# Kernel tuning notes

Measured on AMD Instinct MI355X. Metric: run time of the kernel, lower is better.

Reference implementation:

```python
import jax, jax.numpy as jnp
import numpy as np

N_NODES = 100000
N_EDGES = 1600000
NUM_FEATURES = 256
HIDDEN = 128
NUM_CLASSES = 40


def setup_inputs() -> dict:
    key = jax.random.key(0)
    k1, k2, k3, k4, k5, k6 = jax.random.split(key, 6)
    x = jax.random.normal(k1, (N_NODES, NUM_FEATURES), dtype=jnp.float32)
    edge_index = jax.random.randint(k2, (2, N_EDGES), 0, N_NODES, dtype=jnp.int64)
    # Glorot-like init for weights, zeros-like small bias
    W1 = jax.random.normal(k3, (NUM_FEATURES, HIDDEN), dtype=jnp.float32) / np.sqrt(NUM_FEATURES)
    b1 = jax.random.normal(k4, (HIDDEN,), dtype=jnp.float32) * 0.01
    W2 = jax.random.normal(k5, (HIDDEN, NUM_CLASSES), dtype=jnp.float32) / np.sqrt(HIDDEN)
    b2 = jax.random.normal(k6, (NUM_CLASSES,), dtype=jnp.float32) * 0.01
    return {"x": x, "edge_index": edge_index, "W1": W1, "b1": b1, "W2": W2, "b2": b2}


def _gcn_norm(edge_index, n_nodes):
    # Add self loops, compute symmetric normalization D^-1/2 (A+I) D^-1/2.
    loops = jnp.arange(n_nodes, dtype=edge_index.dtype)
    src = jnp.concatenate([edge_index[0], loops])  # [E + N]
    dst = jnp.concatenate([edge_index[1], loops])
    ones = jnp.ones(src.shape[0], dtype=jnp.float32)
    deg = jax.ops.segment_sum(ones, dst, num_segments=n_nodes)  # in-degree incl. self loop
    dinv = jnp.where(deg > 0, jax.lax.rsqrt(deg), 0.0)
    norm = dinv[src] * dinv[dst]  # [E + N]
    return src, dst, norm


def _gcn_conv(x, src, dst, norm, W, b, n_nodes):
    h = x @ W                       # [N, out] transform first (PyG GCNConv)
    msg = h[src] * norm[:, None]    # [E+N, out] gather + scale
    out = jax.ops.segment_sum(msg, dst, num_segments=n_nodes)  # scatter-add
    return out + b


def reference(x, edge_index, W1, b1, W2, b2):
    n = x.shape[0]
    src, dst, norm = _gcn_norm(edge_index, n)
    h = jax.nn.relu(_gcn_conv(x, src, dst, norm, W1, b1, n))
    # dropout is identity in eval mode
    h = _gcn_conv(h, src, dst, norm, W2, b2, n)
    return jax.nn.log_softmax(h, axis=1)
```

## Files before the change

kernel.cpp:

```cpp
#include <hip/hip_runtime.h>
#include <hip/hip_bf16.h>
#include <math.h>

#define NN 100000
#define NE 1600000
#define NF 256
#define NH 128
#define NC 40
#define NCP 64
#define NC2 48

#define NBINS     ((NN + 255) / 256)
#define BIN_CAP   5120
#define CHUNK_A   4096
#define NB_A      ((NE + CHUNK_A - 1) / CHUNK_A)
#define GEMM1_NB  ((NN + 127) / 128)

#define OFF_CURSOR  200128
#define OFF_DINV    300160
#define OFF_H       3600192
#define OFF_W1T     10000192
#define OFF_W2T     10016576
#define OFF_EBIN    16400192
#define OFF_EREC4   18402112
#define OFF_H2P     20404032

using f32x4  = __attribute__((ext_vector_type(4))) float;
using bf16x8 = __attribute__((ext_vector_type(8))) short;

__device__ inline float2 cvt2(unsigned u) {
    float2 f;
    f.x = __uint_as_float(u << 16);
    f.y = __uint_as_float(u & 0xffff0000u);
    return f;
}

__device__ inline short bfbits(float f) {
    __hip_bfloat16 h = __float2bfloat16(f);
    return *reinterpret_cast<short*>(&h);
}

__device__ inline unsigned pk2(float lo, float hi) {
    return (unsigned)(unsigned short)bfbits(lo) | ((unsigned)(unsigned short)bfbits(hi) << 16);
}

__global__ void initk(int* __restrict__ bin_cursor,
                      const float* __restrict__ W1, __hip_bfloat16* __restrict__ W1t,
                      const float* __restrict__ W2, __hip_bfloat16* __restrict__ W2t) {
    int t = blockIdx.x * blockDim.x + threadIdx.x;
    if (t < NBINS) bin_cursor[t] = t * BIN_CAP;
    if (t < NH * NF) {
        int n = t >> 8;
        int k = t & (NF - 1);
        W1t[t] = __float2bfloat16(W1[(size_t)k * NH + n]);
    }
    if (t < NCP * NH) {
        int n = t >> 7;
        int k = t & (NH - 1);
        W2t[t] = __float2bfloat16((n < NC) ? W2[(size_t)k * NC + n] : 0.f);
    }
}

__global__ __launch_bounds__(1024, 2) void gemm1_passA(
        const int* __restrict__ ei, int* __restrict__ bin_cursor,
        int* __restrict__ ebin,
        const float* __restrict__ X, const __hip_bfloat16* __restrict__ W1t,
        __hip_bfloat16* __restrict__ H) {
    __shared__ __align__(16) int smem[8192];

    const int bi = blockIdx.x / 3;
    const int br = blockIdx.x % 3;

    if (br == 1) {
        int* hist  = smem;
        int* rbase = smem + NBINS;
        int e0 = bi * CHUNK_A;
        int e1 = e0 + CHUNK_A; if (e1 > NE) e1 = NE;
        for (int j = threadIdx.x; j < NBINS; j += 1024) hist[j] = 0;
        __syncthreads();
        for (int p = e0 + threadIdx.x; p < e1; p += 1024)
            atomicAdd(&hist[ei[NE + p] >> 8], 1);
        __syncthreads();
        for (int j = threadIdx.x; j < NBINS; j += 1024) {
            int c = hist[j];
            rbase[j] = c ? atomicAdd(&bin_cursor[j], c) : 0;
        }
        __syncthreads();
        for (int p = e0 + threadIdx.x; p < e1; p += 1024) {
            int s = ei[p];
            int d = ei[NE + p];
            int bb = d >> 8;
            int pos = atomicAdd(&rbase[bb], 1);
            if (pos < (bb + 1) * BIN_CAP)
                ebin[pos] = s | ((d & 255) << 17);
        }
        return;
    }

    short* As = (short*)smem;
    short* Bs = (short*)smem + 8192;

    const int tid  = threadIdx.x;
    const int wave = tid >> 6;
    const int lane = tid & 63;
    const int quad = lane >> 4;
    const int l16  = lane & 15;
    const int wy = wave >> 1, wx = wave & 1;
    const int m0 = (bi * 2 + (br == 2 ? 1 : 0)) * 128;

    const int xrow = tid >> 3, xc4 = tid & 7;
    int gr = m0 + xrow; if (gr > NN - 1) gr = NN - 1;
    const float* xbase = X + (size_t)gr * NF + xc4 * 4;
    const int xdst = xrow * 32 + xc4 * 4;

    f32x4 acc[4] = {};

    auto stageB = [&](int d, int kk) {
        if (wave < 8) {
            int n = tid >> 2, cc = tid & 3;
            const __hip_bfloat16* gp = W1t + (size_t)n * NF + kk + cc * 8;
            __builtin_amdgcn_global_load_lds(
                (const __attribute__((address_space(1))) void*)gp,
                (__attribute__((address_space(3))) void*)&Bs[d * 4096 + wave * 512],
                16, 0, 0);
        }
    };

    {
        f32x4 xr = *(const f32x4*)xbase;
        stageB(0, 0);
        uint2 wpk;
        wpk.x = pk2(xr.x, xr.y);
        wpk.y = pk2(xr.z, xr.w);
        *reinterpret_cast<uint2*>(&As[xdst]) = wpk;
    }
    __syncthreads();

    int cur = 0;
    #pragma unroll
    for (int k0 = 0; k0 < NF; k0 += 32) {
        const bool more = (k0 + 32 < NF);
        f32x4 xn;
        if (more) {
            xn = *(const f32x4*)(xbase + k0 + 32);
            stageB(cur ^ 1, k0 + 32);
        }

        bf16x8 a_frag = *(const bf16x8*)&As[cur * 4096 + (wy * 16 + l16) * 32 + quad * 8];
        bf16x8 b_frag[4];
        #pragma unroll
        for (int ni = 0; ni < 4; ++ni)
            b_frag[ni] = *(const bf16x8*)&Bs[cur * 4096 + (wx * 64 + ni * 16 + l16) * 32 + quad * 8];
        #pragma unroll
        for (int ni = 0; ni < 4; ++ni)
            acc[ni] = __builtin_amdgcn_mfma_f32_16x16x32_bf16(
                a_frag, b_frag[ni], acc[ni], 0, 0, 0);

        if (more) {
            uint2 wpk;
            wpk.x = pk2(xn.x, xn.y);
            wpk.y = pk2(xn.z, xn.w);
            *reinterpret_cast<uint2*>(&As[(cur ^ 1) * 4096 + xdst]) = wpk;
        }
        __syncthreads();
        cur ^= 1;
    }

    #pragma unroll
    for (int v = 0; v < 4; ++v) {
        int r = m0 + wy * 16 + quad * 4 + v;
        if (r < NN) {
            #pragma unroll
            for (int ni = 0; ni < 4; ++ni) {
                int c = wx * 64 + ni * 16 + l16;
                H[(size_t)r * NH + c] = __float2bfloat16(acc[ni][v]);
            }
        }
    }
}

__global__ __launch_bounds__(512) void buildK2(const int* __restrict__ ebin,
                                               const int* __restrict__ bin_cursor,
                                               int2* __restrict__ offr,
                                               float* __restrict__ dinv,
                                               int* __restrict__ erec4) {
    __shared__ int ecache[BIN_CAP];
    __shared__ int hist[256];
    __shared__ int scn[256];
    __shared__ int wsum4[4];

    const int b   = blockIdx.x;
    const int tid = threadIdx.x;
    const int n0  = b << 8;
    const int nodes = (NN - n0 > 256) ? 256 : (NN - n0);
    const int base = b * BIN_CAP;
    int cnt = bin_cursor[b] - base;
    if (cnt > BIN_CAP) cnt = BIN_CAP;

    for (int j = tid; j < 256; j += 512) hist[j] = 0;
    __syncthreads();

    for (int p = tid; p < cnt; p += 512) {
        int e = ebin[base + p];
        ecache[p] = e;
        atomicAdd(&hist[e >> 17], 1);
    }
    __syncthreads();

    int v = 0, s = 0;
    const int lane = tid & 63, wave = tid >> 6;
    if (tid < 256) {
        v = hist[tid];
        s = v;
        #pragma unroll
        for (int off = 1; off < 64; off <<= 1) {
            int u = __shfl_up(s, off, 64);
            if (lane >= off) s += u;
        }
        if (lane == 63) wsum4[wave] = s;
    }
    __syncthreads();
    if (tid == 0) {
        int a = 0;
        #pragma unroll
        for (int w = 0; w < 4; ++w) { int t = wsum4[w]; wsum4[w] = a; a += t; }
    }
    __syncthreads();
    if (tid < 256) {
        int excl = (s - v) + wsum4[wave];
        scn[tid] = excl;
        if (tid < nodes) {
            offr[n0 + tid] = make_int2(base + excl, base + excl + v);
            dinv[n0 + tid] = rsqrtf((float)v + 1.0f);
        }
    }
    __syncthreads();

    for (int p = tid; p < cnt; p += 512) {
        int e = ecache[p];
        int dl = e >> 17;
        int pos = atomicAdd(&scn[dl], 1);
        if (pos < BIN_CAP) erec4[base + pos] = e & 0x1FFFF;
    }
}

__global__ __launch_bounds__(1024, 2) void agg1_gemm2(
        const int2* __restrict__ offr, const int* __restrict__ erec4,
        const float* __restrict__ dinv, const __hip_bfloat16* __restrict__ H,
        const float* __restrict__ b1, const __hip_bfloat16* __restrict__ W2t,
        __hip_bfloat16* __restrict__ H2p) {
    __shared__ __align__(16) short As[128 * 128];
    const int tid  = threadIdx.x;
    const int wave = tid >> 6;
    const int lane = tid & 63;
    const int quad = lane >> 4;
    const int l16  = lane & 15;
    const int grp  = tid >> 4;
    const int m0   = blockIdx.x * 128;
    const char* Hb = (const char*)H;
    const unsigned lb = (unsigned)(l16 << 4);

    #pragma unroll 1
    for (int rd = 0; rd < 2; ++rd) {
        int nl = rd * 64 + grp;
        int node = m0 + nl;
        if (node < NN) {
            int2 be = offr[node];
            int beg = be.x, end = be.y;
            float dls = dinv[node];
            float ac[8] = {};
            for (int p = beg; p < end; p += 4) {
                int s0 = erec4[p];
                int s1 = (p + 1 < end) ? erec4[p + 1] : 0;
                int s2 = (p + 2 < end) ? erec4[p + 2] : 0;
                int s3 = (p + 3 < end) ? erec4[p + 3] : 0;
                float w0 = dinv[s0];
                float w1 = (p + 1 < end) ? dinv[s1] : 0.f;
                float w2 = (p + 2 < end) ? dinv[s2] : 0.f;
                float w3 = (p + 3 < end) ? dinv[s3] : 0.f;
                uint4 h0 = *(const uint4*)(Hb + (((unsigned)s0) << 8) + lb);
                uint4 h1 = *(const uint4*)(Hb + (((unsigned)s1) << 8) + lb);
                uint4 h2 = *(const uint4*)(Hb + (((unsigned)s2) << 8) + lb);
                uint4 h3 = *(const uint4*)(Hb + (((unsigned)s3) << 8) + lb);
                #define ACC8(hv, ww) { \
                    float2 q0 = cvt2(hv.x), q1 = cvt2(hv.y), q2 = cvt2(hv.z), q3 = cvt2(hv.w); \
                    ac[0] += q0.x * (ww); ac[1] += q0.y * (ww); \
                    ac[2] += q1.x * (ww); ac[3] += q1.y * (ww); \
                    ac[4] += q2.x * (ww); ac[5] += q2.y * (ww); \
                    ac[6] += q3.x * (ww); ac[7] += q3.y * (ww); }
                ACC8(h0, w0) ACC8(h1, w1) ACC8(h2, w2) ACC8(h3, w3)
                #undef ACC8
            }
            float sl = dls * dls;
            uint4 hs = *(const uint4*)(Hb + (((unsigned)node) << 8) + lb);
            float2 s0f = cvt2(hs.x), s1f = cvt2(hs.y), s2f = cvt2(hs.z), s3f = cvt2(hs.w);
            const float4* bb = reinterpret_cast<const float4*>(b1 + l16 * 8);
            float4 ba = bb[0], bc = bb[1];
            float o0 = fmaxf(ac[0] * dls + s0f.x * sl + ba.x, 0.f);
            float o1 = fmaxf(ac[1] * dls + s0f.y * sl + ba.y, 0.f);
            float o2 = fmaxf(ac[2] * dls + s1f.x * sl + ba.z, 0.f);
            float o3 = fmaxf(ac[3] * dls + s1f.y * sl + ba.w, 0.f);
            float o4 = fmaxf(ac[4] * dls + s2f.x * sl + bc.x, 0.f);
            float o5 = fmaxf(ac[5] * dls + s2f.y * sl + bc.y, 0.f);
            float o6 = fmaxf(ac[6] * dls + s3f.x * sl + bc.z, 0.f);
            float o7 = fmaxf(ac[7] * dls + s3f.y * sl + bc.w, 0.f);
            uint4 ov;
            ov.x = pk2(o0, o1);
            ov.y = pk2(o2, o3);
            ov.z = pk2(o4, o5);
            ov.w = pk2(o6, o7);
            unsigned cb = lb ^ (((unsigned)nl & 7u) << 4);
            *reinterpret_cast<uint4*>((char*)As + nl * 256 + cb) = ov;
        }
    }

    bf16x8 bfr[4][3];
    if (wave < 8) {
        #pragma unroll
        for (int ks = 0; ks < 4; ++ks)
            #pragma unroll
            for (int ni = 0; ni < 3; ++ni)
                bfr[ks][ni] = *(const bf16x8*)(W2t + (size_t)(ni * 16 + l16) * NH + ks * 32 + quad * 8);
    }

    __syncthreads();
    if (wave >= 8) return;

    f32x4 acc2[3] = {};
    #pragma unroll
    for (int ks = 0; ks < 4; ++ks) {
        int row = wave * 16 + l16;
        unsigned cb = ((unsigned)(ks * 64 + quad * 16)) ^ (((unsigned)row & 7u) << 4);
        bf16x8 afr = *(const bf16x8*)((const char*)As + row * 256 + cb);
        #pragma unroll
        for (int ni = 0; ni < 3; ++ni)
            acc2[ni] = __builtin_amdgcn_mfma_f32_16x16x32_bf16(
                afr, bfr[ks][ni], acc2[ni], 0, 0, 0);
    }

    #pragma unroll
    for (int v = 0; v < 4; ++v) {
        int r = m0 + wave * 16 + quad * 4 + v;
        if (r < NN) {
            #pragma unroll
            for (int ni = 0; ni < 3; ++ni) {
                int c = ni * 16 + l16;
                H2p[(size_t)r * NC2 + c] = __float2bfloat16(acc2[ni][v]);
            }
        }
    }
}

__global__ void agg2_lsm(const int2* __restrict__ offr, const int* __restrict__ erec4,
                         const float* __restrict__ dinv, const __hip_bfloat16* __restrict__ H2p,
                         const float* __restrict__ b2, float* __restrict__ out) {
    int node = (blockIdx.x * blockDim.x + threadIdx.x) >> 4;
    if (node >= NN) return;
    int l16 = threadIdx.x & 15;
    const char* Hb = (const char*)H2p;
    const bool lv = (l16 < 12);
    const unsigned lo = (unsigned)(l16 * 8);
    const uint2 zz = make_uint2(0u, 0u);
    float a0 = 0.f, a1 = 0.f, a2 = 0.f, a3 = 0.f;
    int2 be = offr[node];
    int beg = be.x, end = be.y;
    float di = dinv[node];
    for (int p = beg; p < end; p += 8) {
        int s[8]; float w[8]; uint2 h[8];
        #pragma unroll
        for (int j = 0; j < 8; ++j) s[j] = (p + j < end) ? erec4[p + j] : 0;
        #pragma unroll
        for (int j = 0; j < 8; ++j) w[j] = (p + j < end) ? dinv[s[j]] : 0.f;
        #pragma unroll
        for (int j = 0; j < 8; ++j) h[j] = lv ? *(const uint2*)(Hb + (unsigned)s[j] * 96u + lo) : zz;
        #pragma unroll
        for (int j = 0; j < 8; ++j) {
            float2 q0 = cvt2(h[j].x), q1 = cvt2(h[j].y);
            a0 += q0.x * w[j]; a1 += q0.y * w[j];
            a2 += q1.x * w[j]; a3 += q1.y * w[j];
        }
    }
    float v0, v1, v2, v3;
    bool valid = (l16 < 10);
    if (valid) {
        float sl = di * di;
        uint2 hs = *(const uint2*)(Hb + (unsigned)node * 96u + lo);
        float2 s0f = cvt2(hs.x), s1f = cvt2(hs.y);
        float4 bb = *reinterpret_cast<const float4*>(b2 + l16 * 4);
        v0 = a0 * di + s0f.x * sl + bb.x;
        v1 = a1 * di + s0f.y * sl + bb.y;
        v2 = a2 * di + s1f.x * sl + bb.z;
        v3 = a3 * di + s1f.y * sl + bb.w;
    } else {
        v0 = v1 = v2 = v3 = -INFINITY;
    }
    float m = fmaxf(fmaxf(v0, v1), fmaxf(v2, v3));
    #pragma unroll
    for (int off = 8; off; off >>= 1) m = fmaxf(m, __shfl_xor(m, off, 64));
    float ex = expf(v0 - m) + expf(v1 - m) + expf(v2 - m) + expf(v3 - m);
    #pragma unroll
    for (int off = 8; off; off >>= 1) ex += __shfl_xor(ex, off, 64);
    float ls = logf(ex);
    if (valid) {
        float4 o;
        o.x = v0 - m - ls; o.y = v1 - m - ls;
        o.z = v2 - m - ls; o.w = v3 - m - ls;
        *reinterpret_cast<float4*>(out + (size_t)node * NC + l16 * 4) = o;
    }
}

extern "C" void kernel_launch(void* const* d_in, const int* in_sizes, int n_in,
                              void* d_out, int out_size, void* d_ws, size_t ws_size,
                              hipStream_t stream) {
    const float* x  = (const float*)d_in[0];
    const int*   ei = (const int*)d_in[1];
    const float* W1 = (const float*)d_in[2];
    const float* b1 = (const float*)d_in[3];
    const float* W2 = (const float*)d_in[4];
    const float* b2 = (const float*)d_in[5];
    float* out = (float*)d_out;

    int* wsb = (int*)d_ws;
    int2*  offr       = (int2*)wsb;
    int*   bin_cursor = wsb + OFF_CURSOR;
    float* dinv       = (float*)(wsb + OFF_DINV);
    __hip_bfloat16* H   = (__hip_bfloat16*)(wsb + OFF_H);
    __hip_bfloat16* W1t = (__hip_bfloat16*)(wsb + OFF_W1T);
    __hip_bfloat16* W2t = (__hip_bfloat16*)(wsb + OFF_W2T);
    int* ebin  = wsb + OFF_EBIN;
    int* erec4 = wsb + OFF_EREC4;
    __hip_bfloat16* H2p = (__hip_bfloat16*)(wsb + OFF_H2P);

    initk<<<(NH * NF + 255) / 256, 256, 0, stream>>>(bin_cursor, W1, W1t, W2, W2t);

    gemm1_passA<<<GEMM1_NB + NB_A, 1024, 0, stream>>>(ei, bin_cursor, ebin, x, W1t, H);

    buildK2<<<NBINS, 512, 0, stream>>>(ebin, bin_cursor, offr, dinv, erec4);

    agg1_gemm2<<<(NN + 127) / 128, 1024, 0, stream>>>(offr, erec4, dinv, H, b1, W2t, H2p);

    {
        long long threads = (long long)NN * 16;
        agg2_lsm<<<(unsigned)((threads + 255) / 256), 256, 0, stream>>>(
            offr, erec4, dinv, H2p, b2, out);
    }
}
```

Before: 315.4 us.

## Widen GEMM1 K-step with swizzled LDS, split H2 into aligned tables, enlarge buildK2

GEMM1 now stages 64-wide K tiles with an XOR-swizzled LDS layout, and all 16 waves issue the W1 direct-to-LDS loads. This halves the barrier count and aims to cut LDS bank conflicts, at the cost of doubled shared memory (64KB) in a kernel declared with launch_bounds(1024,2). The layer-2 features are split into a 64-byte table holding 32 columns and a 16-byte table holding 8 columns, so gathers in agg2 hit aligned, cache-line-friendly rows instead of 96-byte rows. buildK2 runs with 1024 threads instead of 512.

```diff
diff --git a/kernel.cpp b/kernel.cpp
--- a/kernel.cpp
+++ b/kernel.cpp
@@ -8,7 +8,6 @@
 #define NH 128
 #define NC 40
 #define NCP 64
-#define NC2 48
 
 #define NBINS     ((NN + 255) / 256)
 #define BIN_CAP   5120
@@ -23,7 +22,8 @@
 #define OFF_W2T     10016576
 #define OFF_EBIN    16400192
 #define OFF_EREC4   18402112
-#define OFF_H2P     20404032
+#define OFF_H2A     20404032
+#define OFF_H2B     22004032
 
 using f32x4  = __attribute__((ext_vector_type(4))) float;
 using bf16x8 = __attribute__((ext_vector_type(8))) short;
@@ -66,7 +66,7 @@
         int* __restrict__ ebin,
         const float* __restrict__ X, const __hip_bfloat16* __restrict__ W1t,
         __hip_bfloat16* __restrict__ H) {
-    __shared__ __align__(16) int smem[8192];
+    __shared__ __align__(16) int smem[16384];
 
     const int bi = blockIdx.x / 3;
     const int br = blockIdx.x % 3;
@@ -98,7 +98,7 @@
     }
 
     short* As = (short*)smem;
-    short* Bs = (short*)smem + 8192;
+    short* Bs = (short*)smem + 16384;
 
     const int tid  = threadIdx.x;
     const int wave = tid >> 6;
@@ -108,59 +108,64 @@
     const int wy = wave >> 1, wx = wave & 1;
     const int m0 = (bi * 2 + (br == 2 ? 1 : 0)) * 128;
 
-    const int xrow = tid >> 3, xc4 = tid & 7;
-    int gr = m0 + xrow; if (gr > NN - 1) gr = NN - 1;
-    const float* xbase = X + (size_t)gr * NF + xc4 * 4;
-    const int xdst = xrow * 32 + xc4 * 4;
+    const int srow = tid >> 3;
+    const int scl  = (tid & 7) ^ (srow & 7);
+    int gr = m0 + srow; if (gr > NN - 1) gr = NN - 1;
+    const float* xbase = X + (size_t)gr * NF + scl * 8;
+    const __hip_bfloat16* wbase = W1t + (size_t)srow * NF + scl * 8;
+    const int ldst = tid * 8;
 
     f32x4 acc[4] = {};
 
     auto stageB = [&](int d, int kk) {
-        if (wave < 8) {
-            int n = tid >> 2, cc = tid & 3;
-            const __hip_bfloat16* gp = W1t + (size_t)n * NF + kk + cc * 8;
-            __builtin_amdgcn_global_load_lds(
-                (const __attribute__((address_space(1))) void*)gp,
-                (__attribute__((address_space(3))) void*)&Bs[d * 4096 + wave * 512],
-                16, 0, 0);
-        }
+        __builtin_amdgcn_global_load_lds(
+            (const __attribute__((address_space(1))) void*)(wbase + kk),
+            (__attribute__((address_space(3))) void*)&Bs[d * 8192 + ldst],
+            16, 0, 0);
     };
 
     {
-        f32x4 xr = *(const f32x4*)xbase;
+        f32x4 x0 = *(const f32x4*)xbase;
+        f32x4 x1 = *(const f32x4*)(xbase + 4);
         stageB(0, 0);
-        uint2 wpk;
-        wpk.x = pk2(xr.x, xr.y);
-        wpk.y = pk2(xr.z, xr.w);
-        *reinterpret_cast<uint2*>(&As[xdst]) = wpk;
+        uint4 w;
+        w.x = pk2(x0.x, x0.y); w.y = pk2(x0.z, x0.w);
+        w.z = pk2(x1.x, x1.y); w.w = pk2(x1.z, x1.w);
+        *reinterpret_cast<uint4*>(&As[ldst]) = w;
     }
     __syncthreads();
 
     int cur = 0;
     #pragma unroll
-    for (int k0 = 0; k0 < NF; k0 += 32) {
-        const bool more = (k0 + 32 < NF);
-        f32x4 xn;
+    for (int k0 = 0; k0 < NF; k0 += 64) {
+        const bool more = (k0 + 64 < NF);
+        f32x4 x0, x1;
         if (more) {
-            xn = *(const f32x4*)(xbase + k0 + 32);
-            stageB(cur ^ 1, k0 + 32);
-        }
-
-        bf16x8 a_frag = *(const bf16x8*)&As[cur * 4096 + (wy * 16 + l16) * 32 + quad * 8];
-        bf16x8 b_frag[4];
-        #pragma unroll
-        for (int ni = 0; ni < 4; ++ni)
-            b_frag[ni] = *(const bf16x8*)&Bs[cur * 4096 + (wx * 64 + ni * 16 + l16) * 32 + quad * 8];
-        #pragma unroll
-        for (int ni = 0; ni < 4; ++ni)
-            acc[ni] = __builtin_amdgcn_mfma_f32_16x16x32_bf16(
-                a_frag, b_frag[ni], acc[ni], 0, 0, 0);
+            x0 = *(const f32x4*)(xbase + k0 + 64);
+            x1 = *(const f32x4*)(xbase + k0 + 68);
+            stageB(cur ^ 1, k0 + 64);
+        }
+
+        #pragma unroll
+        for (int ks = 0; ks < 2; ++ks) {
+            const int ar = wy * 16 + l16;
+            const int ac = (ks * 4 + quad) ^ (ar & 7);
+            bf16x8 a_frag = *(const bf16x8*)&As[cur * 8192 + ar * 64 + ac * 8];
+            #pragma unroll
+            for (int ni = 0; ni < 4; ++ni) {
+                const int brr = wx * 64 + ni * 16 + l16;
+                const int bc  = (ks * 4 + quad) ^ (brr & 7);
+                bf16x8 b_frag = *(const bf16x8*)&Bs[cur * 8192 + brr * 64 + bc * 8];
+                acc[ni] = __builtin_amdgcn_mfma_f32_16x16x32_bf16(
+                    a_frag, b_frag, acc[ni], 0, 0, 0);
+            }
+        }
 
         if (more) {
-            uint2 wpk;
-            wpk.x = pk2(xn.x, xn.y);
-            wpk.y = pk2(xn.z, xn.w);
-            *reinterpret_cast<uint2*>(&As[(cur ^ 1) * 4096 + xdst]) = wpk;
+            uint4 w;
+            w.x = pk2(x0.x, x0.y); w.y = pk2(x0.z, x0.w);
+            w.z = pk2(x1.x, x1.y); w.w = pk2(x1.z, x1.w);
+            *reinterpret_cast<uint4*>(&As[(cur ^ 1) * 8192 + ldst]) = w;
         }
         __syncthreads();
         cur ^= 1;
@@ -179,11 +184,11 @@
     }
 }
 
-__global__ __launch_bounds__(512) void buildK2(const int* __restrict__ ebin,
-                                               const int* __restrict__ bin_cursor,
-                                               int2* __restrict__ offr,
-                                               float* __restrict__ dinv,
-                                               int* __restrict__ erec4) {
+__global__ __launch_bounds__(1024) void buildK2(const int* __restrict__ ebin,
+                                                const int* __restrict__ bin_cursor,
+                                                int2* __restrict__ offr,
+                                                float* __restrict__ dinv,
+                                                int* __restrict__ erec4) {
     __shared__ int ecache[BIN_CAP];
     __shared__ int hist[256];
     __shared__ int scn[256];
@@ -197,10 +202,10 @@
     int cnt = bin_cursor[b] - base;
     if (cnt > BIN_CAP) cnt = BIN_CAP;
 
-    for (int j = tid; j < 256; j += 512) hist[j] = 0;
-    __syncthreads();
-
-    for (int p = tid; p < cnt; p += 512) {
+    if (tid < 256) hist[tid] = 0;
+    __syncthreads();
+
+    for (int p = tid; p < cnt; p += 1024) {
         int e = ebin[base + p];
         ecache[p] = e;
         atomicAdd(&hist[e >> 17], 1);
@@ -236,7 +241,7 @@
     }
     __syncthreads();
 
-    for (int p = tid; p < cnt; p += 512) {
+    for (int p = tid; p < cnt; p += 1024) {
         int e = ecache[p];
         int dl = e >> 17;
         int pos = atomicAdd(&scn[dl], 1);
@@ -248,7 +253,7 @@
         const int2* __restrict__ offr, const int* __restrict__ erec4,
         const float* __restrict__ dinv, const __hip_bfloat16* __restrict__ H,
         const float* __restrict__ b1, const __hip_bfloat16* __restrict__ W2t,
-        __hip_bfloat16* __restrict__ H2p) {
+        __hip_bfloat16* __restrict__ H2a, __hip_bfloat16* __restrict__ H2b) {
     __shared__ __align__(16) short As[128 * 128];
     const int tid  = threadIdx.x;
     const int wave = tid >> 6;
@@ -343,23 +348,26 @@
         int r = m0 + wave * 16 + quad * 4 + v;
         if (r < NN) {
             #pragma unroll
-            for (int ni = 0; ni < 3; ++ni) {
-                int c = ni * 16 + l16;
-                H2p[(size_t)r * NC2 + c] = __float2bfloat16(acc2[ni][v]);
-            }
+            for (int ni = 0; ni < 2; ++ni)
+                H2a[(size_t)r * 32 + ni * 16 + l16] = __float2bfloat16(acc2[ni][v]);
+            if (l16 < 8)
+                H2b[(size_t)r * 8 + l16] = __float2bfloat16(acc2[2][v]);
         }
     }
 }
 
 __global__ void agg2_lsm(const int2* __restrict__ offr, const int* __restrict__ erec4,
-                         const float* __restrict__ dinv, const __hip_bfloat16* __restrict__ H2p,
+                         const float* __restrict__ dinv, const __hip_bfloat16* __restrict__ H2a,
+                         const __hip_bfloat16* __restrict__ H2b,
                          const float* __restrict__ b2, float* __restrict__ out) {
     int node = (blockIdx.x * blockDim.x + threadIdx.x) >> 4;
     if (node >= NN) return;
     int l16 = threadIdx.x & 15;
-    const char* Hb = (const char*)H2p;
-    const bool lv = (l16 < 12);
-    const unsigned lo = (unsigned)(l16 * 8);
+    const bool inA = (l16 < 8);
+    const bool act = (l16 < 10);
+    const char* tb = inA ? (const char*)H2a : (const char*)H2b;
+    const unsigned rmul = inA ? 64u : 16u;
+    const unsigned off  = inA ? (unsigned)(l16 * 8) : (unsigned)((l16 - 8) * 8);
     const uint2 zz = make_uint2(0u, 0u);
     float a0 = 0.f, a1 = 0.f, a2 = 0.f, a3 = 0.f;
     int2 be = offr[node];
@@ -372,7 +380,7 @@
         #pragma unroll
         for (int j = 0; j < 8; ++j) w[j] = (p + j < end) ? dinv[s[j]] : 0.f;
         #pragma unroll
-        for (int j = 0; j < 8; ++j) h[j] = lv ? *(const uint2*)(Hb + (unsigned)s[j] * 96u + lo) : zz;
+        for (int j = 0; j < 8; ++j) h[j] = act ? *(const uint2*)(tb + (unsigned)s[j] * rmul + off) : zz;
         #pragma unroll
         for (int j = 0; j < 8; ++j) {
             float2 q0 = cvt2(h[j].x), q1 = cvt2(h[j].y);
@@ -381,10 +389,9 @@
         }
     }
     float v0, v1, v2, v3;
-    bool valid = (l16 < 10);
-    if (valid) {
+    if (act) {
         float sl = di * di;
-        uint2 hs = *(const uint2*)(Hb + (unsigned)node * 96u + lo);
+        uint2 hs = *(const uint2*)(tb + (unsigned)node * rmul + off);
         float2 s0f = cvt2(hs.x), s1f = cvt2(hs.y);
         float4 bb = *reinterpret_cast<const float4*>(b2 + l16 * 4);
         v0 = a0 * di + s0f.x * sl + bb.x;
@@ -396,12 +403,12 @@
     }
     float m = fmaxf(fmaxf(v0, v1), fmaxf(v2, v3));
     #pragma unroll
-    for (int off = 8; off; off >>= 1) m = fmaxf(m, __shfl_xor(m, off, 64));
+    for (int off2 = 8; off2; off2 >>= 1) m = fmaxf(m, __shfl_xor(m, off2, 64));
     float ex = expf(v0 - m) + expf(v1 - m) + expf(v2 - m) + expf(v3 - m);
     #pragma unroll
-    for (int off = 8; off; off >>= 1) ex += __shfl_xor(ex, off, 64);
+    for (int off2 = 8; off2; off2 >>= 1) ex += __shfl_xor(ex, off2, 64);
     float ls = logf(ex);
-    if (valid) {
+    if (act) {
         float4 o;
         o.x = v0 - m - ls; o.y = v1 - m - ls;
         o.z = v2 - m - ls; o.w = v3 - m - ls;
@@ -429,19 +436,20 @@
     __hip_bfloat16* W2t = (__hip_bfloat16*)(wsb + OFF_W2T);
     int* ebin  = wsb + OFF_EBIN;
     int* erec4 = wsb + OFF_EREC4;
-    __hip_bfloat16* H2p = (__hip_bfloat16*)(wsb + OFF_H2P);
+    __hip_bfloat16* H2a = (__hip_bfloat16*)(wsb + OFF_H2A);
+    __hip_bfloat16* H2b = (__hip_bfloat16*)(wsb + OFF_H2B);
 
     initk<<<(NH * NF + 255) / 256, 256, 0, stream>>>(bin_cursor, W1, W1t, W2, W2t);
 
     gemm1_passA<<<GEMM1_NB + NB_A, 1024, 0, stream>>>(ei, bin_cursor, ebin, x, W1t, H);
 
-    buildK2<<<NBINS, 512, 0, stream>>>(ebin, bin_cursor, offr, dinv, erec4);
-
-    agg1_gemm2<<<(NN + 127) / 128, 1024, 0, stream>>>(offr, erec4, dinv, H, b1, W2t, H2p);
+    buildK2<<<NBINS, 1024, 0, stream>>>(ebin, bin_cursor, offr, dinv, erec4);
+
+    agg1_gemm2<<<(NN + 127) / 128, 1024, 0, stream>>>(offr, erec4, dinv, H, b1, W2t, H2a, H2b);
 
     {
         long long threads = (long long)NN * 16;
         agg2_lsm<<<(unsigned)((threads + 255) / 256), 256, 0, stream>>>(
-            offr, erec4, dinv, H2p, b2, out);
-    }
-}
+            offr, erec4, dinv, H2a, H2b, b2, out);
+    }
+}
```

Measured after the change: 321.8 us. 1.02x slower.
